# Optimization experiments

Hardware: AMD Instinct MI355X
Metric: run time of the kernel (lower is better)

Reference implementation:

```python
import jax, jax.numpy as jnp
import numpy as np

N, C, W_DIM, H_DIM = 2, 256, 64, 64
HEADS = 4
DH = C // HEADS  # per-head dim for Q,K,V projections
EPS = 1e-5


def _layernorm(x, w, b):
    mu = jnp.mean(x, axis=-1, keepdims=True)
    var = jnp.var(x, axis=-1, keepdims=True)
    return (x - mu) * jax.lax.rsqrt(var + EPS) * w + b


def setup_inputs() -> dict:
    key = jax.random.key(0)
    ks = jax.random.split(key, 12)
    s = 1.0 / np.sqrt(C)
    return {
        "x": jax.random.normal(ks[0], (N, C, W_DIM, H_DIM), dtype=jnp.float32),
        "ln1_w": jnp.ones((C,), jnp.float32),
        "ln1_b": jnp.zeros((C,), jnp.float32),
        # per-head projection weights, laid out for x @ W: [heads, C, DH]
        "WQ": jax.random.normal(ks[1], (HEADS, C, DH), jnp.float32) * s,
        "WK": jax.random.normal(ks[2], (HEADS, C, DH), jnp.float32) * s,
        "WV": jax.random.normal(ks[3], (HEADS, C, DH), jnp.float32) * s,
        "ln2_w": jnp.ones((C,), jnp.float32),
        "ln2_b": jnp.zeros((C,), jnp.float32),
        "W1": jax.random.normal(ks[4], (C, C), jnp.float32) * s,
        "b1": jnp.zeros((C,), jnp.float32),
        "W2": jax.random.normal(ks[5], (C, C), jnp.float32) * s,
        "b2": jnp.zeros((C,), jnp.float32),
    }


def reference(x, ln1_w, ln1_b, WQ, WK, WV, ln2_w, ln2_b, W1, b1, W2, b2):
    n, c, w, h = x.shape
    s = w * h
    # 'n c w h -> n (w h) c'
    r = x.reshape(n, c, s).transpose(0, 2, 1)          # [n, s, c]
    norm = _layernorm(r, ln1_w, ln1_b)
    # all heads at once (original loops over heads)
    Q = jnp.einsum('nsc,hcd->nhsd', norm, WQ)
    K = jnp.einsum('nsc,hcd->nhsd', norm, WK)
    V = jnp.einsum('nsc,hcd->nhsd', norm, WV)
    # scale is 1/sqrt(seq_len) per original (keys.shape[1])
    y = jnp.einsum('nhqd,nhkd->nhqk', Q, K) / jnp.sqrt(jnp.float32(s))
    # QUIRK: softmax over dim=1 of [n, q, k] => the QUERY axis (axis=2 here)
    z = jax.nn.softmax(y, axis=2)
    attn = jnp.einsum('nhqk,nhkd->nhqd', z, V)         # [n, h, s, dh]
    attn_cat = attn.transpose(0, 2, 1, 3).reshape(n, s, c)
    out = attn_cat + r
    out = _layernorm(out, ln2_w, ln2_b)
    out = jax.nn.gelu(out @ W1 + b1, approximate=False) @ W2 + b2
    out = out + attn_cat
    # 'n (w h) c -> n c w h'
    return out.transpose(0, 2, 1).reshape(n, c, w, h)
```

## Files before the change

kernel.cpp:

```cpp
#include <hip/hip_runtime.h>
#include <math.h>

#define SEQ 4096
#define CH  256
#define NHT 8
#define DHD 64

#define QSCALE 0.0225421092f

using bf16x8 = __attribute__((ext_vector_type(8))) short;
using f32x4  = __attribute__((ext_vector_type(4))) float;
typedef unsigned short u16;
typedef unsigned int   u32;

__device__ __forceinline__ u16 f2bf(float f) {
    u32 u = __float_as_uint(f);
    u = (u + 0x7fffu + ((u >> 16) & 1u)) >> 16;
    return (u16)u;
}
__device__ __forceinline__ float bf2f(u16 h) {
    return __uint_as_float(((u32)h) << 16);
}
__device__ __forceinline__ float fexp2(float x) {
    return __builtin_amdgcn_exp2f(x);
}

__global__ __launch_bounds__(256) void k_prep(const float* __restrict__ x,
                                              const float* __restrict__ ln1w,
                                              const float* __restrict__ ln1b,
                                              const float* __restrict__ WQ,
                                              const float* __restrict__ WK,
                                              const float* __restrict__ WV,
                                              const float* __restrict__ W1,
                                              const float* __restrict__ W2,
                                              u16* __restrict__ norm,
                                              u16* __restrict__ BtQKV,
                                              u16* __restrict__ W1t,
                                              u16* __restrict__ W2t)
{
    __shared__ float tile[32][257];
    __shared__ float mu[32], rs[32];
    int bid = blockIdx.x;
    int t = threadIdx.x;
    if (bid < 1280) {
        int id = bid * 256 + t;
        if (id < 768 * 256) {
            int j = id >> 8, c = id & 255;
            int which = j >> 8, h = (j >> 6) & 3, d = j & 63;
            const float* W = (which == 0) ? WQ : (which == 1) ? WK : WV;
            BtQKV[id] = f2bf(W[(h * 256 + c) * 64 + d]);
        } else if (id < 768 * 256 + 65536) {
            int jj = id - 768 * 256;
            int j = jj >> 8, c = jj & 255;
            W1t[jj] = f2bf(W1[c * 256 + j]);
        } else if (id < 768 * 256 + 2 * 65536) {
            int jj = id - 768 * 256 - 65536;
            int j = jj >> 8, c = jj & 255;
            W2t[jj] = f2bf(W2[c * 256 + j]);
        }
        return;
    }
    int b2i = bid - 1280;
    int n = b2i >> 7, s0 = (b2i & 127) * 32;
    int sl = t & 31, cg = t >> 5;
    for (int cc = 0; cc < 256; cc += 8) {
        int c = cc + cg;
        tile[sl][c] = x[(n * 256 + c) * SEQ + s0 + sl];
    }
    __syncthreads();
    int wv = t >> 6, l = t & 63;
    for (int rr = 0; rr < 8; rr++) {
        int s = wv * 8 + rr;
        float a0 = tile[s][l], a1 = tile[s][l + 64], a2 = tile[s][l + 128], a3 = tile[s][l + 192];
        float sm = a0 + a1 + a2 + a3;
        float sq = a0 * a0 + a1 * a1 + a2 * a2 + a3 * a3;
        for (int off = 32; off; off >>= 1) { sm += __shfl_xor(sm, off); sq += __shfl_xor(sq, off); }
        if (l == 0) {
            float m = sm * (1.f / 256.f);
            mu[s] = m;
            rs[s] = rsqrtf(sq * (1.f / 256.f) - m * m + 1e-5f);
        }
    }
    __syncthreads();
    float ww = ln1w[t], bb = ln1b[t];
    for (int s = 0; s < 32; s++) {
        float v = (tile[s][t] - mu[s]) * rs[s] * ww + bb;
        norm[(n * SEQ + s0 + s) * 256 + t] = f2bf(v);
    }
}

__global__ __launch_bounds__(256) void k_qkv(const u16* __restrict__ norm,
                                             const u16* __restrict__ Bt,
                                             u16* __restrict__ Qo,
                                             u16* __restrict__ Ko,
                                             float* __restrict__ Vfo)
{
    int m0 = blockIdx.x * 64, j0 = blockIdx.y * 128;
    int t = threadIdx.x, w = t >> 6, lane = t & 63, quad = lane >> 4, l16 = lane & 15;
    const u16* Ap = norm + (long)(m0 + w * 16 + l16) * 256;
    const u16* Bp = Bt + (long)j0 * 256;
    f32x4 z = {0.f, 0.f, 0.f, 0.f};
    f32x4 acc[8];
    #pragma unroll
    for (int j = 0; j < 8; j++) acc[j] = z;
    #pragma unroll
    for (int kc = 0; kc < 8; kc++) {
        bf16x8 a = *(const bf16x8*)&Ap[kc * 32 + quad * 8];
        #pragma unroll
        for (int j = 0; j < 8; j++) {
            bf16x8 b = *(const bf16x8*)&Bp[(long)(j * 16 + l16) * 256 + kc * 32 + quad * 8];
            acc[j] = __builtin_amdgcn_mfma_f32_16x16x32_bf16(a, b, acc[j], 0, 0, 0);
        }
    }
    #pragma unroll
    for (int j = 0; j < 8; j++) {
        int col = j0 + j * 16 + l16;
        int which = col >> 8, h = (col >> 6) & 3, d = col & 63;
        int m = m0 + w * 16 + quad * 4;
        int n = m >> 12, s = m & 4095;
        if (which == 2) {
            float4 o = make_float4(acc[j][0], acc[j][1], acc[j][2], acc[j][3]);
            *(float4*)&Vfo[((long)(n * 4 + h) * 64 + d) * SEQ + s] = o;
        } else {
            u16* dst = (which == 0) ? Qo : Ko;
            float sc = (which == 0) ? QSCALE : 1.0f;
            #pragma unroll
            for (int r = 0; r < 4; r++)
                dst[((n * 4 + h) * SEQ + s + r) * 64 + d] = f2bf(acc[j][r] * sc);
        }
    }
}

__device__ __forceinline__ void xcd_decode(int s, int& g, int& sub) {
    int xcd = s & 7, m = s >> 3;
    g = xcd * 2 + (m >> 5);
    sub = m & 31;
}
__device__ __forceinline__ void xcd_decode32(int s, int& g, int& sub) {
    int xcd = s & 7, m = s >> 3;
    g = xcd * 4 + (m >> 5);
    sub = m & 31;
}

__global__ __launch_bounds__(256) void k_pass1(const u16* __restrict__ Q,
                                               const u16* __restrict__ Km,
                                               float* __restrict__ D2)
{
    __shared__ float Dred[128];
    int g, sub;
    xcd_decode32(blockIdx.x, g, sub);
    int nh = g & 7, qc = g >> 3, k0 = sub * 128;
    const u16* Qh = Q + (long)nh * SEQ * 64;
    const u16* Kh = Km + (long)nh * SEQ * 64;
    int t = threadIdx.x, w = t >> 6, lane = t & 63, quad = lane >> 4, l16 = lane & 15;
    bf16x8 Kf[8][2];
    #pragma unroll
    for (int i = 0; i < 8; i++) {
        Kf[i][0] = *(const bf16x8*)&Kh[(k0 + i * 16 + l16) * 64 + quad * 8];
        Kf[i][1] = *(const bf16x8*)&Kh[(k0 + i * 16 + l16) * 64 + 32 + quad * 8];
    }
    if (t < 128) Dred[t] = 0.f;
    f32x4 z = {0.f, 0.f, 0.f, 0.f};
    float Dacc[8][4] = {};
    const int qw0 = qc * 1024 + w * 256;

#define P1_LOADQ(B0, B1, ST)                                                  \
    {                                                                         \
        int _q = qw0 + (ST) * 16 + l16;                                       \
        B0 = *(const bf16x8*)&Qh[_q * 64 + quad * 8];                         \
        B1 = *(const bf16x8*)&Qh[_q * 64 + 32 + quad * 8];                    \
    }
#define P1_STEP(B0, B1)                                                       \
    {                                                                         \
        _Pragma("unroll")                                                     \
        for (int i = 0; i < 8; i++) {                                         \
            f32x4 acc = z;                                                    \
            acc = __builtin_amdgcn_mfma_f32_16x16x32_bf16(Kf[i][0], B0, acc, 0, 0, 0); \
            acc = __builtin_amdgcn_mfma_f32_16x16x32_bf16(Kf[i][1], B1, acc, 0, 0, 0); \
            _Pragma("unroll")                                                 \
            for (int r = 0; r < 4; r++) Dacc[i][r] += fexp2(acc[r]);          \
        }                                                                     \
    }

    bf16x8 qa0, qa1, qb0, qb1;
    P1_LOADQ(qa0, qa1, 0)
    P1_LOADQ(qb0, qb1, 1)
    for (int st = 0; st < 16; st += 2) {
        P1_STEP(qa0, qa1)
        if (st + 2 < 16) { P1_LOADQ(qa0, qa1, st + 2) }
        P1_STEP(qb0, qb1)
        if (st + 3 < 16) { P1_LOADQ(qb0, qb1, st + 3) }
    }
#undef P1_LOADQ
#undef P1_STEP

    #pragma unroll
    for (int i = 0; i < 8; i++)
        #pragma unroll
        for (int r = 0; r < 4; r++) {
            float v = Dacc[i][r];
            v += __shfl_xor(v, 1); v += __shfl_xor(v, 2);
            v += __shfl_xor(v, 4); v += __shfl_xor(v, 8);
            Dacc[i][r] = v;
        }
    __syncthreads();
    if (l16 == 0) {
        #pragma unroll
        for (int i = 0; i < 8; i++)
            #pragma unroll
            for (int r = 0; r < 4; r++)
                atomicAdd(&Dred[i * 16 + quad * 4 + r], Dacc[i][r]);
    }
    __syncthreads();
    if (t < 128) D2[((long)(qc * NHT + nh)) * SEQ + k0 + t] = Dred[t];
}

__global__ __launch_bounds__(256) void k_vdiv(const float* __restrict__ Vf,
                                              const float* __restrict__ D2,
                                              u16* __restrict__ Vto)
{
    int b = blockIdx.x;
    int nh = b >> 6, d = b & 63;
    const long QS = (long)NHT * SEQ;
    const float* Dp = D2 + (long)nh * SEQ;
    const float* src = Vf + ((long)nh * 64 + d) * SEQ;
    u16* dst = Vto + ((long)nh * 64 + d) * SEQ;
    int t = threadIdx.x;
    #pragma unroll
    for (int half = 0; half < 2; half++) {
        int k = half * 2048 + t * 8;
        float o[8];
        #pragma unroll
        for (int e = 0; e < 8; e++) {
            float dsum = Dp[k + e] + Dp[QS + k + e] + Dp[2 * QS + k + e] + Dp[3 * QS + k + e];
            o[e] = src[k + e] / dsum;
        }
        uint4 pk;
        pk.x = (u32)f2bf(o[0]) | ((u32)f2bf(o[1]) << 16);
        pk.y = (u32)f2bf(o[2]) | ((u32)f2bf(o[3]) << 16);
        pk.z = (u32)f2bf(o[4]) | ((u32)f2bf(o[5]) << 16);
        pk.w = (u32)f2bf(o[6]) | ((u32)f2bf(o[7]) << 16);
        *(uint4*)&dst[k] = pk;
    }
}

__global__ __launch_bounds__(256, 2) void k_pass2(const u16* __restrict__ Q,
                                                  const u16* __restrict__ Km,
                                                  const u16* __restrict__ Vt,
                                                  float* __restrict__ acat2)
{
    __shared__ __align__(16) u16 lP2[2][4][128][36];
    float (*red)[68] = (float(*)[68])lP2;

    int g, sub;
    xcd_decode(blockIdx.x, g, sub);
    int nh = g & 7, kcid = g >> 3, q0 = sub * 128;
    int n = nh >> 2, h = nh & 3;
    const u16* Qh = Q + (long)nh * SEQ * 64;
    const u16* Kh = Km + (long)nh * SEQ * 64;
    const u16* Vh = Vt + (long)nh * 64 * SEQ;
    int t = threadIdx.x, w = t >> 6, lane = t & 63, quad = lane >> 4, l16 = lane & 15;
    const int kblk = kcid * 2048;
    const int dw = w * 16 + l16;

    bf16x8 Qf[8][2];
    #pragma unroll
    for (int jq = 0; jq < 8; jq++)
        #pragma unroll
        for (int ch = 0; ch < 2; ch++)
            Qf[jq][ch] = *(const bf16x8*)&Qh[(q0 + jq * 16 + l16) * 64 + ch * 32 + quad * 8];

    f32x4 z = {0.f, 0.f, 0.f, 0.f};
    f32x4 acc[8];
    #pragma unroll
    for (int jq = 0; jq < 8; jq++) acc[jq] = z;

#define LOAD_K(KA, I)                                                         \
    {                                                                         \
        int _kb = kblk + (I) * 128 + w * 32;                                  \
        _Pragma("unroll")                                                     \
        for (int ksub = 0; ksub < 2; ksub++) {                                \
            KA[ksub][0] = *(const bf16x8*)&Kh[(_kb + ksub * 16 + l16) * 64 + quad * 8];      \
            KA[ksub][1] = *(const bf16x8*)&Kh[(_kb + ksub * 16 + l16) * 64 + 32 + quad * 8]; \
        }                                                                     \
    }
#define LOAD_V(VB, I)                                                         \
    {                                                                         \
        int _kb = kblk + (I) * 128;                                           \
        _Pragma("unroll")                                                     \
        for (int ks = 0; ks < 4; ks++)                                        \
            VB[ks] = *(const bf16x8*)&Vh[(long)dw * SEQ + _kb + ks * 32 + quad * 8]; \
    }
#define QK_STRIPE(KA, B)                                                      \
    {                                                                         \
        _Pragma("unroll")                                                     \
        for (int ksub = 0; ksub < 2; ksub++) {                                \
            _Pragma("unroll")                                                 \
            for (int jq = 0; jq < 8; jq++) {                                  \
                f32x4 s_ = z;                                                 \
                s_ = __builtin_amdgcn_mfma_f32_16x16x32_bf16(KA[ksub][0], Qf[jq][0], s_, 0, 0, 0); \
                s_ = __builtin_amdgcn_mfma_f32_16x16x32_bf16(KA[ksub][1], Qf[jq][1], s_, 0, 0, 0); \
                u32 e0 = __float_as_uint(fexp2(s_[0]));                       \
                u32 e1 = __float_as_uint(fexp2(s_[1]));                       \
                u32 e2 = __float_as_uint(fexp2(s_[2]));                       \
                u32 e3 = __float_as_uint(fexp2(s_[3]));                       \
                uint2 pk;                                                     \
                pk.x = __builtin_amdgcn_perm(e1, e0, 0x07060302u);            \
                pk.y = __builtin_amdgcn_perm(e3, e2, 0x07060302u);            \
                *(uint2*)&lP2[B][w][jq * 16 + l16][ksub * 16 + quad * 4] = pk; \
            }                                                                 \
        }                                                                     \
    }
#define PV_STRIPE(VB, B)                                                      \
    {                                                                         \
        _Pragma("unroll")                                                     \
        for (int ks = 0; ks < 4; ks++) {                                      \
            _Pragma("unroll")                                                 \
            for (int jq = 0; jq < 8; jq++) {                                  \
                bf16x8 pa = *(const bf16x8*)&lP2[B][ks][jq * 16 + l16][quad * 8]; \
                acc[jq] = __builtin_amdgcn_mfma_f32_16x16x32_bf16(pa, VB[ks], acc[jq], 0, 0, 0); \
            }                                                                 \
        }                                                                     \
    }

    bf16x8 kA0[2][2], kA1[2][2], vb0[4], vb1[4];
    LOAD_K(kA0, 0)
    LOAD_V(vb0, 0)
    LOAD_K(kA1, 1)
    LOAD_V(vb1, 1)

    QK_STRIPE(kA0, 0)
    __syncthreads();
    for (int it = 0; it < 7; it++) {
        int i = it * 2;
        QK_STRIPE(kA1, 1)
        LOAD_K(kA0, i + 2)
        PV_STRIPE(vb0, 0)
        LOAD_V(vb0, i + 2)
        __syncthreads();
        QK_STRIPE(kA0, 0)
        LOAD_K(kA1, i + 3)
        PV_STRIPE(vb1, 1)
        LOAD_V(vb1, i + 3)
        __syncthreads();
    }
    QK_STRIPE(kA1, 1)
    PV_STRIPE(vb0, 0)
    __syncthreads();
    PV_STRIPE(vb1, 1)

#undef LOAD_K
#undef LOAD_V
#undef QK_STRIPE
#undef PV_STRIPE

    #pragma unroll
    for (int jq = 0; jq < 8; jq++)
        #pragma unroll
        for (int r = 0; r < 4; r++)
            red[jq * 16 + quad * 4 + r][dw] = acc[jq][r];
    __syncthreads();
    float* dst = acat2 + (long)kcid * 8192 * 256;
    #pragma unroll
    for (int p = 0; p < 8; p++) {
        int row = p * 16 + (t >> 4);
        int ch = (t & 15) * 4;
        float4 o = *(float4*)&red[row][ch];
        *(float4*)&dst[((long)n * SEQ + q0 + row) * 256 + h * 64 + ch] = o;
    }
}

__global__ __launch_bounds__(256) void k_tail(const float* __restrict__ x,
                                              const float* __restrict__ acat2,
                                              const float* __restrict__ lnw,
                                              const float* __restrict__ lnb,
                                              const u16* __restrict__ W1t,
                                              const float* __restrict__ b1v,
                                              const u16* __restrict__ W2t,
                                              const float* __restrict__ b2v,
                                              float* __restrict__ out)
{
    __shared__ __align__(16) unsigned char smem[16448];
    float (*tile)[257] = (float(*)[257])smem;
    u16 (*lT)[264] = (u16(*)[264])smem;
    __shared__ float aF[16][257];
    __shared__ float mu[16], rs[16];
    __shared__ __align__(16) u16 lH[16][264];

    const long STRIDE = (long)8192 * 256;
    int m0 = blockIdx.x * 16;
    int n = m0 >> 12, s0 = m0 & 4095;
    int t = threadIdx.x, w = t >> 6, lane = t & 63, quad = lane >> 4, l16 = lane & 15;

    {
        int sl = t & 15, cg = t >> 4;
        for (int cc = 0; cc < 256; cc += 16) {
            int c = cc + cg;
            tile[sl][c] = x[(n * 256 + c) * SEQ + s0 + sl];
        }
    }
    __syncthreads();
    for (int s = 0; s < 16; s++) {
        long idx = (long)(m0 + s) * 256 + t;
        float a = acat2[idx] + acat2[idx + STRIDE];
        aF[s][t] = a;
        tile[s][t] += a;
    }
    __syncthreads();
    {
        int l = t & 63;
        for (int rr = 0; rr < 4; rr++) {
            int s = w * 4 + rr;
            float a0 = tile[s][l], a1 = tile[s][l + 64], a2 = tile[s][l + 128], a3 = tile[s][l + 192];
            float sm = a0 + a1 + a2 + a3;
            float sq = a0 * a0 + a1 * a1 + a2 * a2 + a3 * a3;
            for (int off = 32; off; off >>= 1) { sm += __shfl_xor(sm, off); sq += __shfl_xor(sq, off); }
            if (l == 0) {
                float m = sm * (1.f / 256.f);
                mu[s] = m;
                rs[s] = rsqrtf(sq * (1.f / 256.f) - m * m + 1e-5f);
            }
        }
    }
    __syncthreads();
    {
        float ww = lnw[t], bb = lnb[t];
        for (int s = 0; s < 16; s++)
            lH[s][t] = f2bf((tile[s][t] - mu[s]) * rs[s] * ww + bb);
    }
    __syncthreads();

    f32x4 z = {0.f, 0.f, 0.f, 0.f};
    f32x4 acc1[4];
    #pragma unroll
    for (int js = 0; js < 4; js++) acc1[js] = z;
    #pragma unroll
    for (int kc = 0; kc < 8; kc++) {
        bf16x8 b = *(const bf16x8*)&lH[l16][kc * 32 + quad * 8];
        #pragma unroll
        for (int js = 0; js < 4; js++) {
            bf16x8 a = *(const bf16x8*)&W1t[(long)(w * 64 + js * 16 + l16) * 256 + kc * 32 + quad * 8];
            acc1[js] = __builtin_amdgcn_mfma_f32_16x16x32_bf16(a, b, acc1[js], 0, 0, 0);
        }
    }
    #pragma unroll
    for (int js = 0; js < 4; js++) {
        u32 e[4];
        #pragma unroll
        for (int r = 0; r < 4; r++) {
            int j = w * 64 + js * 16 + quad * 4 + r;
            float v = acc1[js][r] + b1v[j];
            float g = 0.5f * v * (1.f + erff(v * 0.70710678118f));
            u32 u = __float_as_uint(g);
            e[r] = u + 0x7fffu + ((u >> 16) & 1u);
        }
        uint2 pk;
        pk.x = __builtin_amdgcn_perm(e[1], e[0], 0x07060302u);
        pk.y = __builtin_amdgcn_perm(e[3], e[2], 0x07060302u);
        *(uint2*)&lT[l16][w * 64 + js * 16 + quad * 4] = pk;
    }
    __syncthreads();
    f32x4 acc2[4];
    #pragma unroll
    for (int cs = 0; cs < 4; cs++) acc2[cs] = z;
    #pragma unroll
    for (int kc = 0; kc < 8; kc++) {
        bf16x8 pa = *(const bf16x8*)&lT[l16][kc * 32 + quad * 8];
        #pragma unroll
        for (int cs = 0; cs < 4; cs++) {
            bf16x8 wb = *(const bf16x8*)&W2t[(long)(w * 64 + cs * 16 + l16) * 256 + kc * 32 + quad * 8];
            acc2[cs] = __builtin_amdgcn_mfma_f32_16x16x32_bf16(pa, wb, acc2[cs], 0, 0, 0);
        }
    }
    #pragma unroll
    for (int cs = 0; cs < 4; cs++) {
        int c = w * 64 + cs * 16 + l16;
        float bj = b2v[c];
        float vv[4];
        #pragma unroll
        for (int r = 0; r < 4; r++)
            vv[r] = acc2[cs][r] + bj + aF[quad * 4 + r][c];
        float4 o = make_float4(vv[0], vv[1], vv[2], vv[3]);
        *(float4*)&out[((long)n * 256 + c) * SEQ + s0 + quad * 4] = o;
    }
}

extern "C" void kernel_launch(void* const* d_in, const int* in_sizes, int n_in,
                              void* d_out, int out_size, void* d_ws, size_t ws_size,
                              hipStream_t stream) {
    const float* x    = (const float*)d_in[0];
    const float* ln1w = (const float*)d_in[1];
    const float* ln1b = (const float*)d_in[2];
    const float* WQ   = (const float*)d_in[3];
    const float* WK   = (const float*)d_in[4];
    const float* WV   = (const float*)d_in[5];
    const float* ln2w = (const float*)d_in[6];
    const float* ln2b = (const float*)d_in[7];
    const float* W1   = (const float*)d_in[8];
    const float* b1   = (const float*)d_in[9];
    const float* W2   = (const float*)d_in[10];
    const float* b2   = (const float*)d_in[11];
    float* out = (float*)d_out;

    char* p = (char*)d_ws;
    u16* norm   = (u16*)p;   p += (size_t)8192 * 256 * 2;
    u16* BtQKV  = (u16*)p;   p += (size_t)768 * 256 * 2;
    u16* W1t    = (u16*)p;   p += (size_t)256 * 256 * 2;
    u16* W2t    = (u16*)p;   p += (size_t)256 * 256 * 2;
    u16* Qb     = (u16*)p;   p += (size_t)NHT * SEQ * 64 * 2;
    u16* Kb     = (u16*)p;   p += (size_t)NHT * SEQ * 64 * 2;
    u16* VtT    = (u16*)p;   p += (size_t)NHT * SEQ * 64 * 2;
    float* D2   = (float*)p; p += (size_t)4 * NHT * SEQ * 4;
    float* acat2= (float*)p; p += (size_t)2 * 8192 * 256 * 4;
    float* Vf   = acat2;

    k_prep<<<1536, 256, 0, stream>>>(x, ln1w, ln1b, WQ, WK, WV, W1, W2,
                                     norm, BtQKV, W1t, W2t);
    k_qkv<<<dim3(128, 6), 256, 0, stream>>>(norm, BtQKV, Qb, Kb, Vf);
    k_pass1<<<1024, 256, 0, stream>>>(Qb, Kb, D2);
    k_vdiv<<<512, 256, 0, stream>>>(Vf, D2, VtT);
    k_pass2<<<512, 256, 0, stream>>>(Qb, Kb, VtT, acat2);
    k_tail<<<512, 256, 0, stream>>>(x, acat2, ln2w, ln2b, W1t, b1, W2t, b2, out);
}
```

Measured before the change: 228.2 us.

## Halve pass2 key stage to 64 and raise occupancy to three blocks per CU

The attention pass2 kernel now processes 64 keys per pipeline stage instead of 128. Each wave computes one 16-key slice of QK^T and writes it into a single shared [128][68] P tile, so LDS use and K/V fragment registers drop enough to allow three blocks per CU; pass1 also gets a three-block launch bound. The intent is more resident waves to hide load and exp latency. In exchange the loop needs twice as many iterations and barriers, and a barrier is added before the output reduction reuses the P buffer.

```diff
diff --git a/kernel.cpp b/kernel.cpp
--- a/kernel.cpp
+++ b/kernel.cpp
@@ -142,9 +142,9 @@
     sub = m & 31;
 }
 
-__global__ __launch_bounds__(256) void k_pass1(const u16* __restrict__ Q,
-                                               const u16* __restrict__ Km,
-                                               float* __restrict__ D2)
+__global__ __launch_bounds__(256, 3) void k_pass1(const u16* __restrict__ Q,
+                                                  const u16* __restrict__ Km,
+                                                  float* __restrict__ D2)
 {
     __shared__ float Dred[128];
     int g, sub;
@@ -244,12 +244,12 @@
     }
 }
 
-__global__ __launch_bounds__(256, 2) void k_pass2(const u16* __restrict__ Q,
+__global__ __launch_bounds__(256, 3) void k_pass2(const u16* __restrict__ Q,
                                                   const u16* __restrict__ Km,
                                                   const u16* __restrict__ Vt,
                                                   float* __restrict__ acat2)
 {
-    __shared__ __align__(16) u16 lP2[2][4][128][36];
+    __shared__ __align__(16) u16 lP2[2][128][68];
     float (*red)[68] = (float(*)[68])lP2;
 
     int g, sub;
@@ -277,53 +277,46 @@
 
 #define LOAD_K(KA, I)                                                         \
     {                                                                         \
-        int _kb = kblk + (I) * 128 + w * 32;                                  \
-        _Pragma("unroll")                                                     \
-        for (int ksub = 0; ksub < 2; ksub++) {                                \
-            KA[ksub][0] = *(const bf16x8*)&Kh[(_kb + ksub * 16 + l16) * 64 + quad * 8];      \
-            KA[ksub][1] = *(const bf16x8*)&Kh[(_kb + ksub * 16 + l16) * 64 + 32 + quad * 8]; \
-        }                                                                     \
+        int _kb = kblk + (I) * 64 + w * 16;                                   \
+        KA[0] = *(const bf16x8*)&Kh[(_kb + l16) * 64 + quad * 8];             \
+        KA[1] = *(const bf16x8*)&Kh[(_kb + l16) * 64 + 32 + quad * 8];        \
     }
 #define LOAD_V(VB, I)                                                         \
     {                                                                         \
-        int _kb = kblk + (I) * 128;                                           \
-        _Pragma("unroll")                                                     \
-        for (int ks = 0; ks < 4; ks++)                                        \
-            VB[ks] = *(const bf16x8*)&Vh[(long)dw * SEQ + _kb + ks * 32 + quad * 8]; \
+        int _kb = kblk + (I) * 64;                                            \
+        VB[0] = *(const bf16x8*)&Vh[(long)dw * SEQ + _kb + quad * 8];         \
+        VB[1] = *(const bf16x8*)&Vh[(long)dw * SEQ + _kb + 32 + quad * 8];    \
     }
 #define QK_STRIPE(KA, B)                                                      \
     {                                                                         \
         _Pragma("unroll")                                                     \
-        for (int ksub = 0; ksub < 2; ksub++) {                                \
-            _Pragma("unroll")                                                 \
-            for (int jq = 0; jq < 8; jq++) {                                  \
-                f32x4 s_ = z;                                                 \
-                s_ = __builtin_amdgcn_mfma_f32_16x16x32_bf16(KA[ksub][0], Qf[jq][0], s_, 0, 0, 0); \
-                s_ = __builtin_amdgcn_mfma_f32_16x16x32_bf16(KA[ksub][1], Qf[jq][1], s_, 0, 0, 0); \
-                u32 e0 = __float_as_uint(fexp2(s_[0]));                       \
-                u32 e1 = __float_as_uint(fexp2(s_[1]));                       \
-                u32 e2 = __float_as_uint(fexp2(s_[2]));                       \
-                u32 e3 = __float_as_uint(fexp2(s_[3]));                       \
-                uint2 pk;                                                     \
-                pk.x = __builtin_amdgcn_perm(e1, e0, 0x07060302u);            \
-                pk.y = __builtin_amdgcn_perm(e3, e2, 0x07060302u);            \
-                *(uint2*)&lP2[B][w][jq * 16 + l16][ksub * 16 + quad * 4] = pk; \
-            }                                                                 \
+        for (int jq = 0; jq < 8; jq++) {                                      \
+            f32x4 s_ = z;                                                     \
+            s_ = __builtin_amdgcn_mfma_f32_16x16x32_bf16(KA[0], Qf[jq][0], s_, 0, 0, 0); \
+            s_ = __builtin_amdgcn_mfma_f32_16x16x32_bf16(KA[1], Qf[jq][1], s_, 0, 0, 0); \
+            u32 e0 = __float_as_uint(fexp2(s_[0]));                           \
+            u32 e1 = __float_as_uint(fexp2(s_[1]));                           \
+            u32 e2 = __float_as_uint(fexp2(s_[2]));                           \
+            u32 e3 = __float_as_uint(fexp2(s_[3]));                           \
+            uint2 pk;                                                         \
+            pk.x = __builtin_amdgcn_perm(e1, e0, 0x07060302u);                \
+            pk.y = __builtin_amdgcn_perm(e3, e2, 0x07060302u);                \
+            *(uint2*)&lP2[B][jq * 16 + l16][w * 16 + quad * 4] = pk;          \
         }                                                                     \
     }
 #define PV_STRIPE(VB, B)                                                      \
     {                                                                         \
         _Pragma("unroll")                                                     \
-        for (int ks = 0; ks < 4; ks++) {                                      \
+        for (int ks = 0; ks < 2; ks++) {                                      \
             _Pragma("unroll")                                                 \
             for (int jq = 0; jq < 8; jq++) {                                  \
-                bf16x8 pa = *(const bf16x8*)&lP2[B][ks][jq * 16 + l16][quad * 8]; \
+                bf16x8 pa = *(const bf16x8*)&lP2[B][jq * 16 + l16][ks * 32 + quad * 8]; \
                 acc[jq] = __builtin_amdgcn_mfma_f32_16x16x32_bf16(pa, VB[ks], acc[jq], 0, 0, 0); \
             }                                                                 \
         }                                                                     \
     }
 
-    bf16x8 kA0[2][2], kA1[2][2], vb0[4], vb1[4];
+    bf16x8 kA0[2], kA1[2], vb0[2], vb1[2];
     LOAD_K(kA0, 0)
     LOAD_V(vb0, 0)
     LOAD_K(kA1, 1)
@@ -331,7 +324,7 @@
 
     QK_STRIPE(kA0, 0)
     __syncthreads();
-    for (int it = 0; it < 7; it++) {
+    for (int it = 0; it < 15; it++) {
         int i = it * 2;
         QK_STRIPE(kA1, 1)
         LOAD_K(kA0, i + 2)
@@ -354,6 +347,7 @@
 #undef QK_STRIPE
 #undef PV_STRIPE
 
+    __syncthreads();
     #pragma unroll
     for (int jq = 0; jq < 8; jq++)
         #pragma unroll
```

Measured after the change: 223.3 us, median of 2. -2.2%, faster.

## Split PV work by key-half and d-half per wave to reuse P fragments

Applied to the files above, without the earlier changes.

In the attention PV stage, each wave now handles two 16-wide d tiles over half of the 128-key stripe, not one d tile over all keys. Each P fragment read from LDS therefore feeds two MFMAs, halving LDS reads of P. The cost is a doubled accumulator register footprint and an extra cross-wave reduction through shared memory with additional barriers. The P buffer layout changes to a padded [128][132] row form, and pass1 gets a minimum-occupancy launch bound of 3.

```diff
diff --git a/kernel.cpp b/kernel.cpp
--- a/kernel.cpp
+++ b/kernel.cpp
@@ -142,9 +142,9 @@
     sub = m & 31;
 }
 
-__global__ __launch_bounds__(256) void k_pass1(const u16* __restrict__ Q,
-                                               const u16* __restrict__ Km,
-                                               float* __restrict__ D2)
+__global__ __launch_bounds__(256, 3) void k_pass1(const u16* __restrict__ Q,
+                                                  const u16* __restrict__ Km,
+                                                  float* __restrict__ D2)
 {
     __shared__ float Dred[128];
     int g, sub;
@@ -249,7 +249,7 @@
                                                   const u16* __restrict__ Vt,
                                                   float* __restrict__ acat2)
 {
-    __shared__ __align__(16) u16 lP2[2][4][128][36];
+    __shared__ __align__(16) u16 lP2[2][128][132];
     float (*red)[68] = (float(*)[68])lP2;
 
     int g, sub;
@@ -261,7 +261,7 @@
     const u16* Vh = Vt + (long)nh * 64 * SEQ;
     int t = threadIdx.x, w = t >> 6, lane = t & 63, quad = lane >> 4, l16 = lane & 15;
     const int kblk = kcid * 2048;
-    const int dw = w * 16 + l16;
+    const int dhalf = w >> 1, khalf = w & 1;
 
     bf16x8 Qf[8][2];
     #pragma unroll
@@ -271,9 +271,11 @@
             Qf[jq][ch] = *(const bf16x8*)&Qh[(q0 + jq * 16 + l16) * 64 + ch * 32 + quad * 8];
 
     f32x4 z = {0.f, 0.f, 0.f, 0.f};
-    f32x4 acc[8];
-    #pragma unroll
-    for (int jq = 0; jq < 8; jq++) acc[jq] = z;
+    f32x4 acc[8][2];
+    #pragma unroll
+    for (int jq = 0; jq < 8; jq++)
+        #pragma unroll
+        for (int jd = 0; jd < 2; jd++) acc[jq][jd] = z;
 
 #define LOAD_K(KA, I)                                                         \
     {                                                                         \
@@ -286,10 +288,12 @@
     }
 #define LOAD_V(VB, I)                                                         \
     {                                                                         \
-        int _kb = kblk + (I) * 128;                                           \
+        int _kb = kblk + (I) * 128 + khalf * 64;                              \
         _Pragma("unroll")                                                     \
-        for (int ks = 0; ks < 4; ks++)                                        \
-            VB[ks] = *(const bf16x8*)&Vh[(long)dw * SEQ + _kb + ks * 32 + quad * 8]; \
+        for (int ks = 0; ks < 2; ks++) {                                      \
+            VB[ks][0] = *(const bf16x8*)&Vh[(long)(dhalf * 32 + l16) * SEQ + _kb + ks * 32 + quad * 8];      \
+            VB[ks][1] = *(const bf16x8*)&Vh[(long)(dhalf * 32 + 16 + l16) * SEQ + _kb + ks * 32 + quad * 8]; \
+        }                                                                     \
     }
 #define QK_STRIPE(KA, B)                                                      \
     {                                                                         \
@@ -307,23 +311,25 @@
                 uint2 pk;                                                     \
                 pk.x = __builtin_amdgcn_perm(e1, e0, 0x07060302u);            \
                 pk.y = __builtin_amdgcn_perm(e3, e2, 0x07060302u);            \
-                *(uint2*)&lP2[B][w][jq * 16 + l16][ksub * 16 + quad * 4] = pk; \
+                *(uint2*)&lP2[B][jq * 16 + l16][w * 32 + ksub * 16 + quad * 4] = pk; \
             }                                                                 \
         }                                                                     \
     }
 #define PV_STRIPE(VB, B)                                                      \
     {                                                                         \
         _Pragma("unroll")                                                     \
-        for (int ks = 0; ks < 4; ks++) {                                      \
+        for (int ks = 0; ks < 2; ks++) {                                      \
             _Pragma("unroll")                                                 \
             for (int jq = 0; jq < 8; jq++) {                                  \
-                bf16x8 pa = *(const bf16x8*)&lP2[B][ks][jq * 16 + l16][quad * 8]; \
-                acc[jq] = __builtin_amdgcn_mfma_f32_16x16x32_bf16(pa, VB[ks], acc[jq], 0, 0, 0); \
+                bf16x8 pa = *(const bf16x8*)&lP2[B][jq * 16 + l16][khalf * 64 + ks * 32 + quad * 8]; \
+                _Pragma("unroll")                                             \
+                for (int jd = 0; jd < 2; jd++)                                \
+                    acc[jq][jd] = __builtin_amdgcn_mfma_f32_16x16x32_bf16(pa, VB[ks][jd], acc[jq][jd], 0, 0, 0); \
             }                                                                 \
         }                                                                     \
     }
 
-    bf16x8 kA0[2][2], kA1[2][2], vb0[4], vb1[4];
+    bf16x8 kA0[2][2], kA1[2][2], vb0[2][2], vb1[2][2];
     LOAD_K(kA0, 0)
     LOAD_V(vb0, 0)
     LOAD_K(kA1, 1)
@@ -354,11 +360,26 @@
 #undef QK_STRIPE
 #undef PV_STRIPE
 
-    #pragma unroll
-    for (int jq = 0; jq < 8; jq++)
-        #pragma unroll
-        for (int r = 0; r < 4; r++)
-            red[jq * 16 + quad * 4 + r][dw] = acc[jq][r];
+    __syncthreads();
+    if (khalf == 0) {
+        #pragma unroll
+        for (int jq = 0; jq < 8; jq++)
+            #pragma unroll
+            for (int jd = 0; jd < 2; jd++)
+                #pragma unroll
+                for (int r = 0; r < 4; r++)
+                    red[jq * 16 + quad * 4 + r][dhalf * 32 + jd * 16 + l16] = acc[jq][jd][r];
+    }
+    __syncthreads();
+    if (khalf == 1) {
+        #pragma unroll
+        for (int jq = 0; jq < 8; jq++)
+            #pragma unroll
+            for (int jd = 0; jd < 2; jd++)
+                #pragma unroll
+                for (int r = 0; r < 4; r++)
+                    red[jq * 16 + quad * 4 + r][dhalf * 32 + jd * 16 + l16] += acc[jq][jd][r];
+    }
     __syncthreads();
     float* dst = acat2 + (long)kcid * 8192 * 256;
     #pragma unroll
```

Measured after the change: 221.1 us. 1.03x faster.
